# Performance work log

Hardware: AMD Instinct MI355X
Metric: run time of the kernel (lower is better)

## Reference

```python
import jax, jax.numpy as jnp
import numpy as np

N_NODES = 100000
N_EDGES = 1600000
IN_DIM, HID_DIM, OUT_DIM = 256, 64, 64


def gcn_conv(x, W, b, row, col, ew):
    """PyG GCNConv: linear transform, add self-loops (weight 1), symmetric
    deg^{-1/2} normalization, gather-scale-scatter_add aggregation, bias."""
    n = x.shape[0]
    x = x @ W  # [N, out]
    loops = jnp.arange(n)
    row_f = jnp.concatenate([row, loops])
    col_f = jnp.concatenate([col, loops])
    ew_f = jnp.concatenate([ew, jnp.ones((n,), x.dtype)])
    deg = jax.ops.segment_sum(ew_f, col_f, num_segments=n)  # [N]
    dinv = jnp.where(deg > 0, jax.lax.rsqrt(deg), jnp.zeros_like(deg))
    norm = dinv[row_f] * ew_f * dinv[col_f]  # [E+N]
    msg = x[row_f] * norm[:, None]  # gather + scale, [E+N, out]
    out = jax.ops.segment_sum(msg, col_f, num_segments=n)  # scatter-add
    return out + b


def setup_inputs() -> dict:
    key = jax.random.key(0)
    k1, k2, k3, k4, k5 = jax.random.split(key, 5)
    x = jax.random.normal(k1, (N_NODES, IN_DIM), dtype=jnp.float32)
    edge_index = jax.random.randint(k2, (2, N_EDGES), 0, N_NODES, dtype=jnp.int64)
    edge_count = jax.random.randint(k3, (N_EDGES, 1), 0, 1000, dtype=jnp.int64)
    W1 = jax.random.normal(k4, (IN_DIM, HID_DIM), dtype=jnp.float32) * (1.0 / np.sqrt(IN_DIM))
    b1 = jnp.zeros((HID_DIM,), jnp.float32)
    W2 = jax.random.normal(k5, (HID_DIM, OUT_DIM), dtype=jnp.float32) * (1.0 / np.sqrt(HID_DIM))
    b2 = jnp.zeros((OUT_DIM,), jnp.float32)
    return {"x": x, "edge_index": edge_index, "edge_count": edge_count,
            "W1": W1, "b1": b1, "W2": W2, "b2": b2}


def reference(x, edge_index, edge_count, W1, b1, W2, b2):
    # edge weight: min-max normalize edge_count (squeezed)
    ec = edge_count[:, 0].astype(jnp.float32)
    ew = (ec - ec.min()) / (ec.max() - ec.min())
    row, col = edge_index[0], edge_index[1]
    h = jax.nn.relu(gcn_conv(x, W1, b1, row, col, ew))
    h = gcn_conv(h, W2, b2, row, col, ew)
    # dropout(p=0.5) is identity in eval mode
    node_embeddings = h
    return node_embeddings, jax.nn.log_softmax(h, axis=-1)
```

## Files before the change

### kernel.cpp

```cpp
#include <hip/hip_runtime.h>
#include <climits>

#define ROW_BITS 17
#define ROW_MASK ((1u << ROW_BITS) - 1)
#define MAXDEG 64
#define EPB 2048
#define BKT_SHIFT 9
#define BKT_NODES 512
#define NBK_MAX 256
#define SW 200

__device__ __forceinline__ unsigned short f2bf(float f) {
  unsigned u = __float_as_uint(f);
  u = (u + 0x7fffu + ((u >> 16) & 1u)) >> 16;
  return (unsigned short)u;
}
__device__ __forceinline__ float bf_lo(unsigned d) { return __uint_as_float(d << 16); }
__device__ __forceinline__ float bf_hi(unsigned d) { return __uint_as_float(d & 0xffff0000u); }

__device__ __forceinline__ void gload16(const float* g, float* l) {
  __builtin_amdgcn_global_load_lds(
      (const __attribute__((address_space(1))) void*)(g),
      (__attribute__((address_space(3))) void*)(l),
      16, 0, 0);
}

__global__ __launch_bounds__(256) void k_phase1(
    const int* __restrict__ erow, const int* __restrict__ ecol,
    const int* __restrict__ ec,
    unsigned* __restrict__ arena32, unsigned short* __restrict__ arenaN,
    int* __restrict__ bscan, int* __restrict__ mm, int nE, int NBK) {
  __shared__ int cnt[NBK_MAX];
  __shared__ int sc[256];
  __shared__ int ex[NBK_MAX + 1];
  __shared__ int cur[NBK_MAX];
  __shared__ unsigned rec32s[EPB];
  __shared__ unsigned short recNs[EPB];
  __shared__ int sred[8];
  const int blk = blockIdx.x, tid = threadIdx.x;

  for (int i = tid; i < NBK; i += 256) cnt[i] = 0;
  __syncthreads();

  unsigned c8[8], r32[8];
  int vmin = INT_MAX, vmax = INT_MIN;
  #pragma unroll
  for (int k = 0; k < 8; ++k) {
    int e = blk * EPB + k * 256 + tid;
    if (e < nE) {
      int col = ecol[e], row = erow[e], w = ec[e];
      c8[k] = (unsigned)col;
      r32[k] = (unsigned)row | ((unsigned)w << ROW_BITS);
      vmin = min(vmin, w); vmax = max(vmax, w);
      atomicAdd(&cnt[col >> BKT_SHIFT], 1);
    } else c8[k] = 0xFFFFFFFFu;
  }
  __syncthreads();

  sc[tid] = (tid < NBK) ? cnt[tid] : 0;
  __syncthreads();
  #pragma unroll
  for (int o = 1; o < 256; o <<= 1) {
    int v = sc[tid];
    int vv = (tid >= o) ? sc[tid - o] : 0;
    __syncthreads();
    sc[tid] = v + vv;
    __syncthreads();
  }
  if (tid < NBK) { int e0 = tid ? sc[tid - 1] : 0; ex[tid] = e0; cur[tid] = e0; }
  if (tid == 0) ex[NBK] = sc[NBK - 1];
  __syncthreads();

  #pragma unroll
  for (int k = 0; k < 8; ++k) {
    if (c8[k] != 0xFFFFFFFFu) {
      int b = (int)(c8[k] >> BKT_SHIFT);
      int p = atomicAdd(&cur[b], 1);
      rec32s[p] = r32[k];
      recNs[p] = (unsigned short)(c8[k] & (BKT_NODES - 1));
    }
  }
  __syncthreads();

  int total = ex[NBK];
  #pragma unroll
  for (int k = 0; k < 8; ++k) {
    int i = k * 256 + tid;
    if (i < total) {
      arena32[(size_t)blk * EPB + i] = rec32s[i];
      arenaN[(size_t)blk * EPB + i] = recNs[i];
    }
  }
  if (tid <= NBK) bscan[blk * SW + tid] = ex[tid];

  #pragma unroll
  for (int o = 32; o > 0; o >>= 1) {
    vmin = min(vmin, __shfl_xor(vmin, o));
    vmax = max(vmax, __shfl_xor(vmax, o));
  }
  int wid = tid >> 6;
  if ((tid & 63) == 0) { sred[wid] = vmin; sred[4 + wid] = vmax; }
  __syncthreads();
  if (tid == 0) {
    #pragma unroll
    for (int w2 = 1; w2 < 4; ++w2) {
      vmin = min(vmin, sred[w2]);
      vmax = max(vmax, sred[4 + w2]);
    }
    if (vmin != INT_MAX) atomicMax(&mm[0], 0x7FFFFFFF - vmin);
    if (vmax != INT_MIN) atomicMax(&mm[1], vmax);
  }
}

__global__ __launch_bounds__(256) void k_phase2(
    const unsigned* __restrict__ arena32, const unsigned short* __restrict__ arenaN,
    const int* __restrict__ bscan, const int* __restrict__ mm,
    unsigned* __restrict__ packed, float* __restrict__ dinv,
    unsigned* __restrict__ srcw2, int nN, int nB1) {
  __shared__ int lcnt[BKT_NODES];
  __shared__ unsigned lsum[BKT_NODES];
  const int b = blockIdx.x, tid = threadIdx.x;
  const int base = b << BKT_SHIFT;
  const int nod = min(BKT_NODES, nN - base);

  for (int i = tid; i < BKT_NODES; i += 256) { lcnt[i] = 0; lsum[i] = 0u; }
  __syncthreads();

  for (int sb = tid; sb < nB1; sb += 256) {
    int s0 = bscan[sb * SW + b];
    int s1 = bscan[sb * SW + b + 1];
    for (int p = s0; p < s1; ++p) {
      unsigned rv = arena32[(size_t)sb * EPB + p];
      int nl = arenaN[(size_t)sb * EPB + p];
      int rk = atomicAdd(&lcnt[nl], 1);
      if (rk > MAXDEG - 1) rk = MAXDEG - 1;
      srcw2[(size_t)(base + nl) * MAXDEG + rk] = rv;
      atomicAdd(&lsum[nl], rv >> ROW_BITS);
    }
  }
  __syncthreads();

  float mn = (float)(0x7FFFFFFF - mm[0]);
  float rcp = 1.0f / ((float)mm[1] - mn);
  for (int n = tid; n < nod; n += 256) {
    int c = lcnt[n];
    packed[base + n] = (unsigned)c;
    float deg = ((float)lsum[n] - (float)c * mn) * rcp;
    dinv[base + n] = rsqrtf(deg + 1.0f);
  }
}

template<int K>
__global__ __launch_bounds__(256) void k_gemm(const float* __restrict__ A,
                                              const float* __restrict__ W,
                                              unsigned short* __restrict__ outh, int n) {
  constexpr int KSTEPS = K / 32;
  __shared__ float atile[2][128 * 32];
  __shared__ float wtile[2][32 * 64];
  const int tid = threadIdx.x;
  const int wv = tid >> 6;
  const int tr = tid >> 4, tc = tid & 15;
  const int rbase = blockIdx.x * 128;

  auto stageA = [&](int kt, int bb) {
    #pragma unroll
    for (int r = 0; r < 4; ++r) {
      int f = r * 256 + tid;
      int row = f >> 3, c4s = f & 7;
      int c4 = c4s ^ (row & 7);
      int gr = rbase + row; if (gr >= n) gr = n - 1;
      gload16(A + (size_t)gr * K + kt * 32 + c4 * 4,
              &atile[bb][(r * 256 + wv * 64) * 4]);
    }
  };
  auto stageW = [&](int kt, int bb) {
    #pragma unroll
    for (int r = 0; r < 2; ++r) {
      int f = r * 256 + tid;
      int krow = f >> 4, c4 = f & 15;
      gload16(W + (size_t)(kt * 32 + krow) * 64 + c4 * 4,
              &wtile[bb][(r * 256 + wv * 64) * 4]);
    }
  };

  float4 acc[8];
  #pragma unroll
  for (int i = 0; i < 8; ++i) acc[i] = make_float4(0.f, 0.f, 0.f, 0.f);

  stageA(0, 0); stageW(0, 0);
  __syncthreads();
  int cur = 0;
  for (int kt = 0; kt < KSTEPS; ++kt) {
    if (kt + 1 < KSTEPS) { stageA(kt + 1, cur ^ 1); stageW(kt + 1, cur ^ 1); }
    const float* ab = atile[cur];
    const float* wb = wtile[cur];
    #pragma unroll
    for (int k4 = 0; k4 < 8; ++k4) {
      float4 wv0 = *(const float4*)&wb[(k4 * 4 + 0) * 64 + tc * 4];
      float4 wv1 = *(const float4*)&wb[(k4 * 4 + 1) * 64 + tc * 4];
      float4 wv2 = *(const float4*)&wb[(k4 * 4 + 2) * 64 + tc * 4];
      float4 wv3 = *(const float4*)&wb[(k4 * 4 + 3) * 64 + tc * 4];
      #pragma unroll
      for (int i = 0; i < 8; ++i) {
        int row = tr + 16 * i;
        float4 av = *(const float4*)&ab[row * 32 + ((k4 ^ (row & 7)) * 4)];
        acc[i].x = fmaf(av.x, wv0.x, acc[i].x);
        acc[i].y = fmaf(av.x, wv0.y, acc[i].y);
        acc[i].z = fmaf(av.x, wv0.z, acc[i].z);
        acc[i].w = fmaf(av.x, wv0.w, acc[i].w);
        acc[i].x = fmaf(av.y, wv1.x, acc[i].x);
        acc[i].y = fmaf(av.y, wv1.y, acc[i].y);
        acc[i].z = fmaf(av.y, wv1.z, acc[i].z);
        acc[i].w = fmaf(av.y, wv1.w, acc[i].w);
        acc[i].x = fmaf(av.z, wv2.x, acc[i].x);
        acc[i].y = fmaf(av.z, wv2.y, acc[i].y);
        acc[i].z = fmaf(av.z, wv2.z, acc[i].z);
        acc[i].w = fmaf(av.z, wv2.w, acc[i].w);
        acc[i].x = fmaf(av.w, wv3.x, acc[i].x);
        acc[i].y = fmaf(av.w, wv3.y, acc[i].y);
        acc[i].z = fmaf(av.w, wv3.z, acc[i].z);
        acc[i].w = fmaf(av.w, wv3.w, acc[i].w);
      }
    }
    __syncthreads();
    cur ^= 1;
  }
  #pragma unroll
  for (int i = 0; i < 8; ++i) {
    int row = rbase + tr + 16 * i;
    if (row < n) {
      ushort4 o4;
      o4.x = f2bf(acc[i].x); o4.y = f2bf(acc[i].y);
      o4.z = f2bf(acc[i].z); o4.w = f2bf(acc[i].w);
      *(ushort4*)&outh[(size_t)row * 64 + tc * 4] = o4;
    }
  }
}

template<bool FINAL>
__global__ void k_agg(const unsigned* __restrict__ packed,
                      const unsigned* __restrict__ srcw2,
                      const int* __restrict__ mm,
                      const float* __restrict__ dinv,
                      const unsigned short* __restrict__ xwh,
                      const float* __restrict__ b,
                      float* __restrict__ outp, int nN) {
  int node = blockIdx.x * (blockDim.x >> 6) + (threadIdx.x >> 6);
  if (node >= nN) return;
  int lane = threadIdx.x & 63;
  int grp = lane >> 3, sub = lane & 7;
  float mn = (float)(0x7FFFFFFF - mm[0]);
  float rcp = 1.0f / ((float)mm[1] - mn);
  float dc = dinv[node];
  const uint4* xw16 = (const uint4*)xwh;
  float acc[8] = {0.f, 0.f, 0.f, 0.f, 0.f, 0.f, 0.f, 0.f};
  size_t s = (size_t)node * MAXDEG;
  int m = min((int)packed[node], MAXDEG);
  {
    int rsrc = 0;
    float nrmv = 0.f;
    if (lane < m) {
      unsigned rw = srcw2[s + lane];
      rsrc = rw & ROW_MASK;
      nrmv = dinv[rsrc] * (((float)(rw >> ROW_BITS) - mn) * rcp) * dc;
    }
    for (int j = 0; j < m; j += 8) {
      int jj = j + grp;
      int r = __shfl(rsrc, jj);
      float nv = __shfl(nrmv, jj);
      uint4 d = xw16[(size_t)r * 8 + sub];
      acc[0] = fmaf(nv, bf_lo(d.x), acc[0]);
      acc[1] = fmaf(nv, bf_hi(d.x), acc[1]);
      acc[2] = fmaf(nv, bf_lo(d.y), acc[2]);
      acc[3] = fmaf(nv, bf_hi(d.y), acc[3]);
      acc[4] = fmaf(nv, bf_lo(d.z), acc[4]);
      acc[5] = fmaf(nv, bf_hi(d.z), acc[5]);
      acc[6] = fmaf(nv, bf_lo(d.w), acc[6]);
      acc[7] = fmaf(nv, bf_hi(d.w), acc[7]);
    }
  }
  #pragma unroll
  for (int k = 0; k < 8; ++k) acc[k] += __shfl_xor(acc[k], 8);
  #pragma unroll
  for (int k = 0; k < 8; ++k) acc[k] += __shfl_xor(acc[k], 16);
  #pragma unroll
  for (int k = 0; k < 8; ++k) acc[k] += __shfl_xor(acc[k], 32);

  if (lane < 8) {
    uint4 d = xw16[(size_t)node * 8 + sub];
    float sv[8] = {bf_lo(d.x), bf_hi(d.x), bf_lo(d.y), bf_hi(d.y),
                   bf_lo(d.z), bf_hi(d.z), bf_lo(d.w), bf_hi(d.w)};
    float dcc = dc * dc;
    float v[8];
    #pragma unroll
    for (int k = 0; k < 8; ++k) v[k] = acc[k] + dcc * sv[k] + b[sub * 8 + k];
    size_t o0 = (size_t)node * 64 + sub * 8;
    if (FINAL) {
      *(float4*)&outp[o0]     = make_float4(v[0], v[1], v[2], v[3]);
      *(float4*)&outp[o0 + 4] = make_float4(v[4], v[5], v[6], v[7]);
      float mx = v[0];
      #pragma unroll
      for (int k = 1; k < 8; ++k) mx = fmaxf(mx, v[k]);
      #pragma unroll
      for (int o = 1; o < 8; o <<= 1) mx = fmaxf(mx, __shfl_xor(mx, o));
      float e = 0.f;
      #pragma unroll
      for (int k = 0; k < 8; ++k) e += expf(v[k] - mx);
      #pragma unroll
      for (int o = 1; o < 8; o <<= 1) e += __shfl_xor(e, o);
      float ls = mx + logf(e);
      size_t o1 = (size_t)nN * 64 + o0;
      *(float4*)&outp[o1]     = make_float4(v[0] - ls, v[1] - ls, v[2] - ls, v[3] - ls);
      *(float4*)&outp[o1 + 4] = make_float4(v[4] - ls, v[5] - ls, v[6] - ls, v[7] - ls);
    } else {
      #pragma unroll
      for (int k = 0; k < 8; ++k) v[k] = fmaxf(v[k], 0.f);
      *(float4*)&outp[o0]     = make_float4(v[0], v[1], v[2], v[3]);
      *(float4*)&outp[o0 + 4] = make_float4(v[4], v[5], v[6], v[7]);
    }
  }
}

extern "C" void kernel_launch(void* const* d_in, const int* in_sizes, int n_in,
                              void* d_out, int out_size, void* d_ws, size_t ws_size,
                              hipStream_t stream) {
  const float* x  = (const float*)d_in[0];
  const int*   ei = (const int*)d_in[1];
  const int*   ec = (const int*)d_in[2];
  const float* W1 = (const float*)d_in[3];
  const float* b1 = (const float*)d_in[4];
  const float* W2 = (const float*)d_in[5];
  const float* b2 = (const float*)d_in[6];

  int nN = in_sizes[0] / 256;
  int nE = in_sizes[2];
  const int* erow = ei;
  const int* ecol = ei + nE;
  int n64 = nN * 64;

  int nB1 = (nE + EPB - 1) / EPB;
  int NBK = (nN + BKT_NODES - 1) / BKT_NODES;

  auto al4 = [](size_t v) { return (v + 3) & ~(size_t)3; };
  int* wsi = (int*)d_ws;
  int* mm = wsi;
  size_t off = 16;
  unsigned* packed = (unsigned*)(wsi + off);          off = al4(off + (size_t)nN);
  float* dinv   = (float*)(wsi + off);                off = al4(off + nN);
  unsigned* srcw2 = (unsigned*)(wsi + off);           off = al4(off + (size_t)MAXDEG * nN);
  unsigned short* xwh = (unsigned short*)(wsi + off); off = al4(off + 32 * (size_t)nN);
  int* Ustart = wsi + off;
  unsigned* arena32 = (unsigned*)Ustart;
  unsigned short* arenaN = (unsigned short*)(arena32 + (size_t)nB1 * EPB);
  int* bscan = (int*)(arenaN + (size_t)nB1 * EPB);
  float* h1 = (float*)Ustart;
  float* outp = (float*)d_out;

  hipMemsetAsync(d_ws, 0, 64, stream);

  k_phase1<<<nB1, 256, 0, stream>>>(erow, ecol, ec, arena32, arenaN, bscan, mm, nE, NBK);
  k_gemm<256><<<(nN + 127) / 128, 256, 0, stream>>>(x, W1, xwh, nN);
  k_phase2<<<NBK, 256, 0, stream>>>(arena32, arenaN, bscan, mm, packed, dinv,
                                    srcw2, nN, nB1);

  k_agg<false><<<(nN + 3) / 4, 256, 0, stream>>>(packed, srcw2, mm, dinv, xwh, b1, h1, nN);

  k_gemm<64><<<(nN + 127) / 128, 256, 0, stream>>>(h1, W2, xwh, nN);
  k_agg<true><<<(nN + 3) / 4, 256, 0, stream>>>(packed, srcw2, mm, dinv, xwh, b2, outp, nN);
}
```

Baseline: 271.9 us.

## Bucket edges globally with atomic cursors, store hidden layer as bf16, simplify GEMMs

Phase 1 now claims space in per-bucket global arenas with atomic cursors, so phase 2 reads each bucket contiguously with 1024 threads. Before, each bucket block walked roughly 800 per-block scan segments serially. The hidden activations from the first aggregation are written as bf16, and a new dedicated bf16-input GEMM computes the second layer, halving that intermediate traffic. The first GEMM drops LDS double buffering to save shared memory and raise occupancy, which can expose load latency. Buckets hold a fixed capacity (CAP) and overflow records are silently dropped, a correctness risk for skewed graphs.

```diff
diff --git a/kernel.cpp b/kernel.cpp
--- a/kernel.cpp
+++ b/kernel.cpp
@@ -8,7 +8,6 @@
 #define BKT_SHIFT 9
 #define BKT_NODES 512
 #define NBK_MAX 256
-#define SW 200
 
 __device__ __forceinline__ unsigned short f2bf(float f) {
   unsigned u = __float_as_uint(f);
@@ -28,14 +27,17 @@
 __global__ __launch_bounds__(256) void k_phase1(
     const int* __restrict__ erow, const int* __restrict__ ecol,
     const int* __restrict__ ec,
-    unsigned* __restrict__ arena32, unsigned short* __restrict__ arenaN,
-    int* __restrict__ bscan, int* __restrict__ mm, int nE, int NBK) {
+    unsigned* __restrict__ cursors,
+    unsigned* __restrict__ arena32g, unsigned short* __restrict__ arenaNg,
+    int CAP, int* __restrict__ mm, int nE, int NBK) {
   __shared__ int cnt[NBK_MAX];
   __shared__ int sc[256];
   __shared__ int ex[NBK_MAX + 1];
   __shared__ int cur[NBK_MAX];
+  __shared__ int gb[NBK_MAX];
   __shared__ unsigned rec32s[EPB];
   __shared__ unsigned short recNs[EPB];
+  __shared__ unsigned char recB[EPB];
   __shared__ int sred[8];
   const int blk = blockIdx.x, tid = threadIdx.x;
 
@@ -78,7 +80,12 @@
       int p = atomicAdd(&cur[b], 1);
       rec32s[p] = r32[k];
       recNs[p] = (unsigned short)(c8[k] & (BKT_NODES - 1));
-    }
+      recB[p] = (unsigned char)b;
+    }
+  }
+  if (tid < NBK) {
+    int c = cnt[tid];
+    gb[tid] = c ? (int)atomicAdd(&cursors[tid], (unsigned)c) : 0;
   }
   __syncthreads();
 
@@ -87,11 +94,14 @@
   for (int k = 0; k < 8; ++k) {
     int i = k * 256 + tid;
     if (i < total) {
-      arena32[(size_t)blk * EPB + i] = rec32s[i];
-      arenaN[(size_t)blk * EPB + i] = recNs[i];
-    }
-  }
-  if (tid <= NBK) bscan[blk * SW + tid] = ex[tid];
+      int b = recB[i];
+      int pos = gb[b] + (i - ex[b]);
+      if (pos < CAP) {
+        arena32g[(size_t)b * CAP + pos] = rec32s[i];
+        arenaNg[(size_t)b * CAP + pos] = recNs[i];
+      }
+    }
+  }
 
   #pragma unroll
   for (int o = 32; o > 0; o >>= 1) {
@@ -112,37 +122,34 @@
   }
 }
 
-__global__ __launch_bounds__(256) void k_phase2(
-    const unsigned* __restrict__ arena32, const unsigned short* __restrict__ arenaN,
-    const int* __restrict__ bscan, const int* __restrict__ mm,
+__global__ __launch_bounds__(1024) void k_phase2(
+    const unsigned* __restrict__ arena32g, const unsigned short* __restrict__ arenaNg,
+    int CAP, const unsigned* __restrict__ cursors, const int* __restrict__ mm,
     unsigned* __restrict__ packed, float* __restrict__ dinv,
-    unsigned* __restrict__ srcw2, int nN, int nB1) {
+    unsigned* __restrict__ srcw2, int nN) {
   __shared__ int lcnt[BKT_NODES];
   __shared__ unsigned lsum[BKT_NODES];
   const int b = blockIdx.x, tid = threadIdx.x;
   const int base = b << BKT_SHIFT;
   const int nod = min(BKT_NODES, nN - base);
 
-  for (int i = tid; i < BKT_NODES; i += 256) { lcnt[i] = 0; lsum[i] = 0u; }
-  __syncthreads();
-
-  for (int sb = tid; sb < nB1; sb += 256) {
-    int s0 = bscan[sb * SW + b];
-    int s1 = bscan[sb * SW + b + 1];
-    for (int p = s0; p < s1; ++p) {
-      unsigned rv = arena32[(size_t)sb * EPB + p];
-      int nl = arenaN[(size_t)sb * EPB + p];
-      int rk = atomicAdd(&lcnt[nl], 1);
-      if (rk > MAXDEG - 1) rk = MAXDEG - 1;
-      srcw2[(size_t)(base + nl) * MAXDEG + rk] = rv;
-      atomicAdd(&lsum[nl], rv >> ROW_BITS);
-    }
+  for (int i = tid; i < BKT_NODES; i += 1024) { lcnt[i] = 0; lsum[i] = 0u; }
+  __syncthreads();
+
+  int nrec = min((int)cursors[b], CAP);
+  for (int i = tid; i < nrec; i += 1024) {
+    unsigned rv = arena32g[(size_t)b * CAP + i];
+    int nl = arenaNg[(size_t)b * CAP + i];
+    int rk = atomicAdd(&lcnt[nl], 1);
+    if (rk > MAXDEG - 1) rk = MAXDEG - 1;
+    srcw2[(size_t)(base + nl) * MAXDEG + rk] = rv;
+    atomicAdd(&lsum[nl], rv >> ROW_BITS);
   }
   __syncthreads();
 
   float mn = (float)(0x7FFFFFFF - mm[0]);
   float rcp = 1.0f / ((float)mm[1] - mn);
-  for (int n = tid; n < nod; n += 256) {
+  for (int n = tid; n < nod; n += 1024) {
     int c = lcnt[n];
     packed[base + n] = (unsigned)c;
     float deg = ((float)lsum[n] - (float)c * mn) * rcp;
@@ -150,19 +157,23 @@
   }
 }
 
-template<int K>
-__global__ __launch_bounds__(256) void k_gemm(const float* __restrict__ A,
-                                              const float* __restrict__ W,
-                                              unsigned short* __restrict__ outh, int n) {
-  constexpr int KSTEPS = K / 32;
-  __shared__ float atile[2][128 * 32];
-  __shared__ float wtile[2][32 * 64];
+__global__ __launch_bounds__(256) void k_gemm1(const float* __restrict__ A,
+                                               const float* __restrict__ W,
+                                               unsigned short* __restrict__ outh,
+                                               int n) {
+  constexpr int K = 256, KSTEPS = K / 32;
+  __shared__ float atile[128 * 32];
+  __shared__ float wtile[32 * 64];
   const int tid = threadIdx.x;
   const int wv = tid >> 6;
   const int tr = tid >> 4, tc = tid & 15;
   const int rbase = blockIdx.x * 128;
 
-  auto stageA = [&](int kt, int bb) {
+  float4 acc[8];
+  #pragma unroll
+  for (int i = 0; i < 8; ++i) acc[i] = make_float4(0.f, 0.f, 0.f, 0.f);
+
+  for (int kt = 0; kt < KSTEPS; ++kt) {
     #pragma unroll
     for (int r = 0; r < 4; ++r) {
       int f = r * 256 + tid;
@@ -170,40 +181,26 @@
       int c4 = c4s ^ (row & 7);
       int gr = rbase + row; if (gr >= n) gr = n - 1;
       gload16(A + (size_t)gr * K + kt * 32 + c4 * 4,
-              &atile[bb][(r * 256 + wv * 64) * 4]);
-    }
-  };
-  auto stageW = [&](int kt, int bb) {
+              &atile[(r * 256 + wv * 64) * 4]);
+    }
     #pragma unroll
     for (int r = 0; r < 2; ++r) {
       int f = r * 256 + tid;
       int krow = f >> 4, c4 = f & 15;
       gload16(W + (size_t)(kt * 32 + krow) * 64 + c4 * 4,
-              &wtile[bb][(r * 256 + wv * 64) * 4]);
-    }
-  };
-
-  float4 acc[8];
-  #pragma unroll
-  for (int i = 0; i < 8; ++i) acc[i] = make_float4(0.f, 0.f, 0.f, 0.f);
-
-  stageA(0, 0); stageW(0, 0);
-  __syncthreads();
-  int cur = 0;
-  for (int kt = 0; kt < KSTEPS; ++kt) {
-    if (kt + 1 < KSTEPS) { stageA(kt + 1, cur ^ 1); stageW(kt + 1, cur ^ 1); }
-    const float* ab = atile[cur];
-    const float* wb = wtile[cur];
+              &wtile[(r * 256 + wv * 64) * 4]);
+    }
+    __syncthreads();
     #pragma unroll
     for (int k4 = 0; k4 < 8; ++k4) {
-      float4 wv0 = *(const float4*)&wb[(k4 * 4 + 0) * 64 + tc * 4];
-      float4 wv1 = *(const float4*)&wb[(k4 * 4 + 1) * 64 + tc * 4];
-      float4 wv2 = *(const float4*)&wb[(k4 * 4 + 2) * 64 + tc * 4];
-      float4 wv3 = *(const float4*)&wb[(k4 * 4 + 3) * 64 + tc * 4];
+      float4 wv0 = *(const float4*)&wtile[(k4 * 4 + 0) * 64 + tc * 4];
+      float4 wv1 = *(const float4*)&wtile[(k4 * 4 + 1) * 64 + tc * 4];
+      float4 wv2 = *(const float4*)&wtile[(k4 * 4 + 2) * 64 + tc * 4];
+      float4 wv3 = *(const float4*)&wtile[(k4 * 4 + 3) * 64 + tc * 4];
       #pragma unroll
       for (int i = 0; i < 8; ++i) {
         int row = tr + 16 * i;
-        float4 av = *(const float4*)&ab[row * 32 + ((k4 ^ (row & 7)) * 4)];
+        float4 av = *(const float4*)&atile[row * 32 + ((k4 ^ (row & 7)) * 4)];
         acc[i].x = fmaf(av.x, wv0.x, acc[i].x);
         acc[i].y = fmaf(av.x, wv0.y, acc[i].y);
         acc[i].z = fmaf(av.x, wv0.z, acc[i].z);
@@ -223,7 +220,6 @@
       }
     }
     __syncthreads();
-    cur ^= 1;
   }
   #pragma unroll
   for (int i = 0; i < 8; ++i) {
@@ -237,6 +233,81 @@
   }
 }
 
+__global__ __launch_bounds__(256) void k_gemm64h(
+    const unsigned short* __restrict__ A,
+    const float* __restrict__ W,
+    unsigned short* __restrict__ outh, int n) {
+  __shared__ unsigned short atile[128 * 64];
+  __shared__ float wtile[64 * 64];
+  const int tid = threadIdx.x;
+  const int wv = tid >> 6;
+  const int tr = tid >> 4, tc = tid & 15;
+  const int rbase = blockIdx.x * 128;
+
+  #pragma unroll
+  for (int r = 0; r < 4; ++r) {
+    int f = r * 256 + tid;
+    int row = f >> 3, c8s = f & 7;
+    int c8 = c8s ^ (row & 7);
+    int gr = rbase + row; if (gr >= n) gr = n - 1;
+    gload16((const float*)(A + (size_t)gr * 64 + c8 * 8),
+            (float*)&atile[(r * 256 + wv * 64) * 8]);
+  }
+  #pragma unroll
+  for (int r = 0; r < 4; ++r) {
+    int f = r * 256 + tid;
+    int krow = f >> 4, c4 = f & 15;
+    gload16(W + (size_t)krow * 64 + c4 * 4,
+            (float*)&wtile[(r * 256 + wv * 64) * 4]);
+  }
+  __syncthreads();
+
+  float4 acc[8];
+  #pragma unroll
+  for (int i = 0; i < 8; ++i) acc[i] = make_float4(0.f, 0.f, 0.f, 0.f);
+
+  #pragma unroll
+  for (int k8 = 0; k8 < 8; ++k8) {
+    float4 wk[8];
+    #pragma unroll
+    for (int kk = 0; kk < 8; ++kk)
+      wk[kk] = *(const float4*)&wtile[(k8 * 8 + kk) * 64 + tc * 4];
+    #pragma unroll
+    for (int i = 0; i < 8; ++i) {
+      int row = tr + 16 * i;
+      uint4 d = *(const uint4*)&atile[row * 64 + ((k8 ^ (row & 7)) * 8)];
+      float a0 = bf_lo(d.x), a1 = bf_hi(d.x), a2 = bf_lo(d.y), a3 = bf_hi(d.y);
+      float a4 = bf_lo(d.z), a5 = bf_hi(d.z), a6 = bf_lo(d.w), a7 = bf_hi(d.w);
+      acc[i].x = fmaf(a0, wk[0].x, acc[i].x); acc[i].y = fmaf(a0, wk[0].y, acc[i].y);
+      acc[i].z = fmaf(a0, wk[0].z, acc[i].z); acc[i].w = fmaf(a0, wk[0].w, acc[i].w);
+      acc[i].x = fmaf(a1, wk[1].x, acc[i].x); acc[i].y = fmaf(a1, wk[1].y, acc[i].y);
+      acc[i].z = fmaf(a1, wk[1].z, acc[i].z); acc[i].w = fmaf(a1, wk[1].w, acc[i].w);
+      acc[i].x = fmaf(a2, wk[2].x, acc[i].x); acc[i].y = fmaf(a2, wk[2].y, acc[i].y);
+      acc[i].z = fmaf(a2, wk[2].z, acc[i].z); acc[i].w = fmaf(a2, wk[2].w, acc[i].w);
+      acc[i].x = fmaf(a3, wk[3].x, acc[i].x); acc[i].y = fmaf(a3, wk[3].y, acc[i].y);
+      acc[i].z = fmaf(a3, wk[3].z, acc[i].z); acc[i].w = fmaf(a3, wk[3].w, acc[i].w);
+      acc[i].x = fmaf(a4, wk[4].x, acc[i].x); acc[i].y = fmaf(a4, wk[4].y, acc[i].y);
+      acc[i].z = fmaf(a4, wk[4].z, acc[i].z); acc[i].w = fmaf(a4, wk[4].w, acc[i].w);
+      acc[i].x = fmaf(a5, wk[5].x, acc[i].x); acc[i].y = fmaf(a5, wk[5].y, acc[i].y);
+      acc[i].z = fmaf(a5, wk[5].z, acc[i].z); acc[i].w = fmaf(a5, wk[5].w, acc[i].w);
+      acc[i].x = fmaf(a6, wk[6].x, acc[i].x); acc[i].y = fmaf(a6, wk[6].y, acc[i].y);
+      acc[i].z = fmaf(a6, wk[6].z, acc[i].z); acc[i].w = fmaf(a6, wk[6].w, acc[i].w);
+      acc[i].x = fmaf(a7, wk[7].x, acc[i].x); acc[i].y = fmaf(a7, wk[7].y, acc[i].y);
+      acc[i].z = fmaf(a7, wk[7].z, acc[i].z); acc[i].w = fmaf(a7, wk[7].w, acc[i].w);
+    }
+  }
+  #pragma unroll
+  for (int i = 0; i < 8; ++i) {
+    int row = rbase + tr + 16 * i;
+    if (row < n) {
+      ushort4 o4;
+      o4.x = f2bf(acc[i].x); o4.y = f2bf(acc[i].y);
+      o4.z = f2bf(acc[i].z); o4.w = f2bf(acc[i].w);
+      *(ushort4*)&outh[(size_t)row * 64 + tc * 4] = o4;
+    }
+  }
+}
+
 template<bool FINAL>
 __global__ void k_agg(const unsigned* __restrict__ packed,
                       const unsigned* __restrict__ srcw2,
@@ -244,7 +315,9 @@
                       const float* __restrict__ dinv,
                       const unsigned short* __restrict__ xwh,
                       const float* __restrict__ b,
-                      float* __restrict__ outp, int nN) {
+                      float* __restrict__ outp,
+                      unsigned short* __restrict__ outh,
+                      int nN) {
   int node = blockIdx.x * (blockDim.x >> 6) + (threadIdx.x >> 6);
   if (node >= nN) return;
   int lane = threadIdx.x & 63;
@@ -294,8 +367,8 @@
     float v[8];
     #pragma unroll
     for (int k = 0; k < 8; ++k) v[k] = acc[k] + dcc * sv[k] + b[sub * 8 + k];
-    size_t o0 = (size_t)node * 64 + sub * 8;
     if (FINAL) {
+      size_t o0 = (size_t)node * 64 + sub * 8;
       *(float4*)&outp[o0]     = make_float4(v[0], v[1], v[2], v[3]);
       *(float4*)&outp[o0 + 4] = make_float4(v[4], v[5], v[6], v[7]);
       float mx = v[0];
@@ -315,8 +388,12 @@
     } else {
       #pragma unroll
       for (int k = 0; k < 8; ++k) v[k] = fmaxf(v[k], 0.f);
-      *(float4*)&outp[o0]     = make_float4(v[0], v[1], v[2], v[3]);
-      *(float4*)&outp[o0 + 4] = make_float4(v[4], v[5], v[6], v[7]);
+      uint4 o4;
+      o4.x = (unsigned)f2bf(v[0]) | ((unsigned)f2bf(v[1]) << 16);
+      o4.y = (unsigned)f2bf(v[2]) | ((unsigned)f2bf(v[3]) << 16);
+      o4.z = (unsigned)f2bf(v[4]) | ((unsigned)f2bf(v[5]) << 16);
+      o4.w = (unsigned)f2bf(v[6]) | ((unsigned)f2bf(v[7]) << 16);
+      *(uint4*)&outh[(size_t)node * 64 + sub * 8] = o4;
     }
   }
 }
@@ -336,35 +413,38 @@
   int nE = in_sizes[2];
   const int* erow = ei;
   const int* ecol = ei + nE;
-  int n64 = nN * 64;
 
   int nB1 = (nE + EPB - 1) / EPB;
   int NBK = (nN + BKT_NODES - 1) / BKT_NODES;
+  int CAP = nE / NBK + 1024;
 
   auto al4 = [](size_t v) { return (v + 3) & ~(size_t)3; };
   int* wsi = (int*)d_ws;
   int* mm = wsi;
-  size_t off = 16;
+  unsigned* cursors = (unsigned*)(wsi + 16);
+  size_t off = 16 + NBK_MAX;
   unsigned* packed = (unsigned*)(wsi + off);          off = al4(off + (size_t)nN);
   float* dinv   = (float*)(wsi + off);                off = al4(off + nN);
   unsigned* srcw2 = (unsigned*)(wsi + off);           off = al4(off + (size_t)MAXDEG * nN);
   unsigned short* xwh = (unsigned short*)(wsi + off); off = al4(off + 32 * (size_t)nN);
   int* Ustart = wsi + off;
-  unsigned* arena32 = (unsigned*)Ustart;
-  unsigned short* arenaN = (unsigned short*)(arena32 + (size_t)nB1 * EPB);
-  int* bscan = (int*)(arenaN + (size_t)nB1 * EPB);
-  float* h1 = (float*)Ustart;
+  unsigned* arena32g = (unsigned*)Ustart;
+  unsigned short* arenaNg = (unsigned short*)(arena32g + (size_t)NBK * CAP);
+  unsigned short* h1b = (unsigned short*)Ustart;
   float* outp = (float*)d_out;
 
-  hipMemsetAsync(d_ws, 0, 64, stream);
-
-  k_phase1<<<nB1, 256, 0, stream>>>(erow, ecol, ec, arena32, arenaN, bscan, mm, nE, NBK);
-  k_gemm<256><<<(nN + 127) / 128, 256, 0, stream>>>(x, W1, xwh, nN);
-  k_phase2<<<NBK, 256, 0, stream>>>(arena32, arenaN, bscan, mm, packed, dinv,
-                                    srcw2, nN, nB1);
-
-  k_agg<false><<<(nN + 3) / 4, 256, 0, stream>>>(packed, srcw2, mm, dinv, xwh, b1, h1, nN);
-
-  k_gemm<64><<<(nN + 127) / 128, 256, 0, stream>>>(h1, W2, xwh, nN);
-  k_agg<true><<<(nN + 3) / 4, 256, 0, stream>>>(packed, srcw2, mm, dinv, xwh, b2, outp, nN);
-}
+  hipMemsetAsync(d_ws, 0, (16 + NBK_MAX) * 4, stream);
+
+  k_phase1<<<nB1, 256, 0, stream>>>(erow, ecol, ec, cursors, arena32g, arenaNg,
+                                    CAP, mm, nE, NBK);
+  k_gemm1<<<(nN + 127) / 128, 256, 0, stream>>>(x, W1, xwh, nN);
+  k_phase2<<<NBK, 1024, 0, stream>>>(arena32g, arenaNg, CAP, cursors, mm,
+                                     packed, dinv, srcw2, nN);
+
+  k_agg<false><<<(nN + 3) / 4, 256, 0, stream>>>(packed, srcw2, mm, dinv, xwh,
+                                                 b1, nullptr, h1b, nN);
+
+  k_gemm64h<<<(nN + 127) / 128, 256, 0, stream>>>(h1b, W2, xwh, nN);
+  k_agg<true><<<(nN + 3) / 4, 256, 0, stream>>>(packed, srcw2, mm, dinv, xwh,
+                                                b2, outp, nullptr, nN);
+}
```

Measured after the change: 292.9 us. 1.08x slower.
